# Kernel optimization log

Measured on AMD Instinct MI355X. Metric: run time of the kernel, lower is better.

## Reference

```python
import jax, jax.numpy as jnp
import numpy as np

NEG_SLOPE = 0.2  # DGL GATConv default negative_slope


def gat_conv(x, W, attn_l, attn_r, bias, src, dst, n_nodes):
    """DGL-style GATConv. x:[N,F_in], W:[F_in,H*D], attn_l/attn_r/bias:[H,D].
    Returns [N,H,D]."""
    H, D = attn_l.shape
    feat = (x @ W).reshape(n_nodes, H, D)            # projected features
    el = jnp.sum(feat * attn_l, axis=-1)              # [N,H]
    er = jnp.sum(feat * attn_r, axis=-1)              # [N,H]
    e = jax.nn.leaky_relu(el[src] + er[dst], NEG_SLOPE)  # [E,H] per-edge score
    # edge softmax over incoming edges of each dst node (numerically stable)
    m = jax.ops.segment_max(e, dst, num_segments=n_nodes)   # [N,H]
    a = jnp.exp(e - m[dst])
    denom = jax.ops.segment_sum(a, dst, num_segments=n_nodes)
    alpha = a / denom[dst]                            # [E,H]
    msg = feat[src] * alpha[..., None]                # [E,H,D]
    out = jax.ops.segment_sum(msg, dst, num_segments=n_nodes)  # [N,H,D]
    return out + bias


def setup_inputs() -> dict:
    key = jax.random.key(0)
    ks = jax.random.split(key, 12)
    N, E = 50000, 800000
    F_in, D1, H1, F_out = 128, 32, 4, 64
    h = jax.random.normal(ks[0], (N, F_in), dtype=jnp.float32)
    src = jax.random.randint(ks[1], (E,), 0, N, dtype=jnp.int32)
    dst = jax.random.randint(ks[2], (E,), 0, N, dtype=jnp.int32)
    s1 = 1.0 / np.sqrt(F_in)
    s2 = 1.0 / np.sqrt(H1 * D1)
    W1 = jax.random.normal(ks[3], (F_in, H1 * D1), dtype=jnp.float32) * s1
    al1 = jax.random.normal(ks[4], (H1, D1), dtype=jnp.float32) * s1
    ar1 = jax.random.normal(ks[5], (H1, D1), dtype=jnp.float32) * s1
    b1 = jnp.zeros((H1, D1), dtype=jnp.float32)
    W2 = jax.random.normal(ks[6], (H1 * D1, 1 * F_out), dtype=jnp.float32) * s2
    al2 = jax.random.normal(ks[7], (1, F_out), dtype=jnp.float32) * s2
    ar2 = jax.random.normal(ks[8], (1, F_out), dtype=jnp.float32) * s2
    b2 = jnp.zeros((1, F_out), dtype=jnp.float32)
    return {"h": h, "src": src, "dst": dst,
            "W1": W1, "al1": al1, "ar1": ar1, "b1": b1,
            "W2": W2, "al2": al2, "ar2": ar2, "b2": b2}


def reference(h, src, dst, W1, al1, ar1, b1, W2, al2, ar2, b2):
    N = h.shape[0]
    x = gat_conv(h, W1, al1, ar1, b1, src, dst, N)   # [N,H,D]
    x = jax.nn.relu(x.reshape(N, -1))                # flatten heads + ReLU
    # dropout(p=0.2) is identity in eval mode
    x = gat_conv(x, W2, al2, ar2, b2, src, dst, N)   # [N,1,F_out]
    return x.squeeze(1)
```

## Files before the change

kernel.cpp:

```cpp
#include <hip/hip_runtime.h>

#define NEG_SLOPE 0.2f
#define CH 4096
#define DCAP 2048
#define BSTRIDE 1536

__device__ inline unsigned short f2bf(float f) {
    unsigned u = __float_as_uint(f);
    unsigned r = (u + 0x7FFFu + ((u >> 16) & 1u)) >> 16;
    return (unsigned short)r;
}
__device__ inline unsigned pack2bf(float a, float b) {
    return (unsigned)f2bf(a) | ((unsigned)f2bf(b) << 16);
}
__device__ inline float bf2f(unsigned short s) {
    return __uint_as_float(((unsigned)s) << 16);
}
__device__ inline float bf2f_lo(unsigned u) { return __uint_as_float(u << 16); }
__device__ inline float bf2f_hi(unsigned u) { return __uint_as_float(u & 0xFFFF0000u); }
__device__ inline void wave_lds_fence() {
    asm volatile("s_waitcnt lgkmcnt(0)" ::: "memory");
}

__global__ __launch_bounds__(256) void csrP_gemm1_kernel(
    const int* __restrict__ src, const int* __restrict__ dst,
    int* __restrict__ bucket_cursor, unsigned* __restrict__ tmp, int E, int NB,
    int nchunks, const float* __restrict__ h, const float* __restrict__ W1,
    const float* __restrict__ al1, const float* __restrict__ ar1,
    unsigned short* __restrict__ feat1b, float* __restrict__ el1,
    float* __restrict__ er1, int N) {
    __shared__ __align__(16) int smem[8192];
    const int tid = threadIdx.x;
    if ((int)blockIdx.x < nchunks) {
        int* lh = smem;
        int* lex = smem + 1024;
        int* gbase_sh = smem + 2048;
        int* psum = smem + 3072;
        unsigned* sortedv = (unsigned*)(smem + 3328);
        const int base_e = blockIdx.x * CH;
        const int cnt_e = min(CH, E - base_e);
        for (int i = tid; i < 1024; i += 256) lh[i] = 0;
        __syncthreads();
        for (int i = tid; i < cnt_e; i += 256) atomicAdd(&lh[dst[base_e + i] >> 6], 1);
        __syncthreads();
        int s0 = lh[tid * 4], s1 = lh[tid * 4 + 1], s2 = lh[tid * 4 + 2],
            s3 = lh[tid * 4 + 3];
        int tot = s0 + s1 + s2 + s3;
        psum[tid] = tot;
        __syncthreads();
        for (int off = 1; off < 256; off <<= 1) {
            int t = (tid >= off) ? psum[tid - off] : 0;
            __syncthreads();
            psum[tid] += t;
            __syncthreads();
        }
        int ebase = psum[tid] - tot;
        lex[tid * 4] = ebase;
        lex[tid * 4 + 1] = ebase + s0;
        lex[tid * 4 + 2] = ebase + s0 + s1;
        lex[tid * 4 + 3] = ebase + s0 + s1 + s2;
        for (int b = tid; b < NB; b += 256) {
            int c = lh[b];
            gbase_sh[b] = c ? atomicAdd(&bucket_cursor[b], c) : 0;
        }
        __syncthreads();
        for (int i = tid; i < 1024; i += 256) lh[i] = 0;
        __syncthreads();
        for (int i = tid; i < cnt_e; i += 256) {
            int e = base_e + i;
            int d = dst[e];
            unsigned b = (unsigned)d >> 6;
            int r = atomicAdd(&lh[b], 1);
            sortedv[lex[b] + r] =
                (b << 22) | ((unsigned)(d & 63) << 16) | (unsigned)(src[e] & 0xFFFF);
        }
        __syncthreads();
        for (int i = tid; i < cnt_e; i += 256) {
            unsigned v = sortedv[i];
            int b = v >> 22;
            int pos = gbase_sh[b] + (i - lex[b]);
            if (pos < BSTRIDE)
                tmp[(size_t)b * BSTRIDE + pos] = v;
        }
    } else {
        float* xs = (float*)smem;
        const int row0 = ((int)blockIdx.x - nchunks) * 64;
        {
            const float4* s4 = (const float4*)h;
            float4* d4 = (float4*)xs;
            int base4 = row0 * 32;
            int tot4 = N * 32;
            for (int i = tid; i < 2048; i += 256)
                if (base4 + i < tot4) d4[i] = s4[base4 + i];
        }
        __syncthreads();
        const int lane = tid & 31;
        const int c0 = lane * 4;
        const int r0 = (tid >> 5) * 8;
        float acc[8][4] = {};
#pragma unroll 4
        for (int k = 0; k < 128; ++k) {
            float4 w = *(const float4*)(W1 + k * 128 + c0);
#pragma unroll
            for (int r = 0; r < 8; ++r) {
                float x = xs[(r0 + r) * 128 + k];
                acc[r][0] = fmaf(x, w.x, acc[r][0]);
                acc[r][1] = fmaf(x, w.y, acc[r][1]);
                acc[r][2] = fmaf(x, w.z, acc[r][2]);
                acc[r][3] = fmaf(x, w.w, acc[r][3]);
            }
        }
        float4 alv = *(const float4*)(al1 + c0);
        float4 arv = *(const float4*)(ar1 + c0);
#pragma unroll
        for (int r = 0; r < 8; ++r) {
            int row = row0 + r0 + r;
            if (row < N) {
                ushort4 fb;
                fb.x = f2bf(acc[r][0]);
                fb.y = f2bf(acc[r][1]);
                fb.z = f2bf(acc[r][2]);
                fb.w = f2bf(acc[r][3]);
                *(ushort4*)(feat1b + (size_t)row * 128 + c0) = fb;
                float pl = acc[r][0] * alv.x + acc[r][1] * alv.y + acc[r][2] * alv.z +
                           acc[r][3] * alv.w;
                float pr = acc[r][0] * arv.x + acc[r][1] * arv.y + acc[r][2] * arv.z +
                           acc[r][3] * arv.w;
#pragma unroll
                for (int off = 4; off >= 1; off >>= 1) {
                    pl += __shfl_xor(pl, off, 32);
                    pr += __shfl_xor(pr, off, 32);
                }
                if ((lane & 7) == 0) {
                    el1[row * 4 + (lane >> 3)] = pl;
                    er1[row * 4 + (lane >> 3)] = pr;
                }
            }
        }
    }
}

__global__ __launch_bounds__(256) void bucketD_kernel(const unsigned* __restrict__ tmp,
                                                      const int* __restrict__ bucket_cursor,
                                                      int* __restrict__ srcs,
                                                      int* __restrict__ row_beg,
                                                      int* __restrict__ row_end, int N) {
    __shared__ unsigned sval[DCAP];
    __shared__ int ssrc[DCAP];
    __shared__ int dh[64], dex[64], dcur[64];
    const int b = blockIdx.x;
    const int tid = threadIdx.x;
    const int gb = b * BSTRIDE;
    const int cnt = min(bucket_cursor[b], BSTRIDE);
    if (tid < 64) dh[tid] = 0;
    __syncthreads();
    for (int i = tid; i < cnt; i += 256) {
        unsigned v = tmp[gb + i];
        sval[i] = v;
        atomicAdd(&dh[(v >> 16) & 63], 1);
    }
    __syncthreads();
    if (tid < 64) {
        int v = dh[tid], inc = v;
        for (int off = 1; off < 64; off <<= 1) {
            int t = __shfl_up(inc, off, 64);
            if (tid >= off) inc += t;
        }
        dex[tid] = inc - v;
        dcur[tid] = 0;
        int dglob = b * 64 + tid;
        if (dglob < N) {
            row_beg[dglob] = gb + inc - v;
            row_end[dglob] = gb + inc;
        }
    }
    __syncthreads();
    for (int i = tid; i < cnt; i += 256) {
        unsigned val = sval[i];
        int dl = (val >> 16) & 63;
        int r = atomicAdd(&dcur[dl], 1);
        ssrc[dex[dl] + r] = (int)(val & 0xFFFFu);
    }
    __syncthreads();
    for (int i = tid; i < cnt; i += 256) srcs[gb + i] = ssrc[i];
}

__global__ __launch_bounds__(256) void gemm2_fused(const unsigned short* __restrict__ out1b,
                                                   const float* __restrict__ W2,
                                                   const float* __restrict__ al2,
                                                   const float* __restrict__ ar2,
                                                   unsigned short* __restrict__ feat2b,
                                                   float* __restrict__ el2,
                                                   float* __restrict__ er2, int N) {
    __shared__ float xs[64 * 128];
    const int tid = threadIdx.x;
    const int row0 = blockIdx.x * 64;
    {
        const uint4* s8 = (const uint4*)out1b;
        int base8 = row0 * 16;
        int tot8 = N * 16;
        for (int i = tid; i < 1024; i += 256)
            if (base8 + i < tot8) {
                uint4 v = s8[base8 + i];
                float* o = xs + i * 8;
                o[0] = bf2f_lo(v.x);
                o[1] = bf2f_hi(v.x);
                o[2] = bf2f_lo(v.y);
                o[3] = bf2f_hi(v.y);
                o[4] = bf2f_lo(v.z);
                o[5] = bf2f_hi(v.z);
                o[6] = bf2f_lo(v.w);
                o[7] = bf2f_hi(v.w);
            }
    }
    __syncthreads();
    const int lane = tid & 15;
    const int c0 = lane * 4;
    const int r0 = (tid >> 4) * 4;
    float acc[4][4] = {};
#pragma unroll 4
    for (int k = 0; k < 128; ++k) {
        float4 w = *(const float4*)(W2 + k * 64 + c0);
#pragma unroll
        for (int r = 0; r < 4; ++r) {
            float x = xs[(r0 + r) * 128 + k];
            acc[r][0] = fmaf(x, w.x, acc[r][0]);
            acc[r][1] = fmaf(x, w.y, acc[r][1]);
            acc[r][2] = fmaf(x, w.z, acc[r][2]);
            acc[r][3] = fmaf(x, w.w, acc[r][3]);
        }
    }
    float4 alv = *(const float4*)(al2 + c0);
    float4 arv = *(const float4*)(ar2 + c0);
#pragma unroll
    for (int r = 0; r < 4; ++r) {
        int row = row0 + r0 + r;
        if (row < N) {
            ushort4 fb;
            fb.x = f2bf(acc[r][0]);
            fb.y = f2bf(acc[r][1]);
            fb.z = f2bf(acc[r][2]);
            fb.w = f2bf(acc[r][3]);
            *(ushort4*)(feat2b + (size_t)row * 64 + c0) = fb;
            float pl = acc[r][0] * alv.x + acc[r][1] * alv.y + acc[r][2] * alv.z +
                       acc[r][3] * alv.w;
            float pr = acc[r][0] * arv.x + acc[r][1] * arv.y + acc[r][2] * arv.z +
                       acc[r][3] * arv.w;
#pragma unroll
            for (int off = 8; off >= 1; off >>= 1) {
                pl += __shfl_xor(pl, off, 16);
                pr += __shfl_xor(pr, off, 16);
            }
            if (lane == 0) {
                el2[row] = pl;
                er2[row] = pr;
            }
        }
    }
}

__global__ __launch_bounds__(256) void gather1_kernel(const int* __restrict__ row_beg,
                                                      const int* __restrict__ row_end,
                                                      const int* __restrict__ srcs,
                                                      const float* __restrict__ el1,
                                                      const float* __restrict__ er1,
                                                      const unsigned short* __restrict__ feat1b,
                                                      const float* __restrict__ b1,
                                                      unsigned short* __restrict__ out1b,
                                                      int N) {
    __shared__ int s_sh[4][64];
    __shared__ float a_sh[4][256];
    const int tid = threadIdx.x;
    const int w = tid >> 6;
    const int lane = tid & 63;
    const int d = blockIdx.x * 4 + w;
    if (d >= N) return;
    const int beg = row_beg[d], end = row_end[d];
    const int q = lane >> 4;
    const int l16 = lane & 15;
    const int c0 = l16 * 8;
    const int h = l16 >> 2;
    float4 er4 = *(const float4*)(er1 + (size_t)d * 4);
    float acc[8] = {}, bcc[8] = {};
    float den = 0.f;
    for (int k0 = beg; k0 < end; k0 += 64) {
        const int M = min(64, end - k0);
        if (lane < M) {
            int s = srcs[k0 + lane];
            s_sh[w][lane] = s;
            float4 el4 = *(const float4*)(el1 + (size_t)s * 4);
            float v0 = el4.x + er4.x;
            float v1 = el4.y + er4.y;
            float v2 = el4.z + er4.z;
            float v3 = el4.w + er4.w;
            v0 = v0 > 0.f ? v0 : NEG_SLOPE * v0;
            v1 = v1 > 0.f ? v1 : NEG_SLOPE * v1;
            v2 = v2 > 0.f ? v2 : NEG_SLOPE * v2;
            v3 = v3 > 0.f ? v3 : NEG_SLOPE * v3;
            a_sh[w][lane * 4 + 0] = __expf(v0);
            a_sh[w][lane * 4 + 1] = __expf(v1);
            a_sh[w][lane * 4 + 2] = __expf(v2);
            a_sh[w][lane * 4 + 3] = __expf(v3);
        }
        wave_lds_fence();
        int e = q;
        for (; e + 4 < M; e += 8) {
            int s0 = s_sh[w][e], s1 = s_sh[w][e + 4];
            float a0 = a_sh[w][e * 4 + h];
            float a1 = a_sh[w][(e + 4) * 4 + h];
            uint4 f0 = *(const uint4*)(feat1b + (size_t)s0 * 128 + c0);
            uint4 f1 = *(const uint4*)(feat1b + (size_t)s1 * 128 + c0);
            den += a0 + a1;
            acc[0] = fmaf(bf2f_lo(f0.x), a0, acc[0]);
            acc[1] = fmaf(bf2f_hi(f0.x), a0, acc[1]);
            acc[2] = fmaf(bf2f_lo(f0.y), a0, acc[2]);
            acc[3] = fmaf(bf2f_hi(f0.y), a0, acc[3]);
            acc[4] = fmaf(bf2f_lo(f0.z), a0, acc[4]);
            acc[5] = fmaf(bf2f_hi(f0.z), a0, acc[5]);
            acc[6] = fmaf(bf2f_lo(f0.w), a0, acc[6]);
            acc[7] = fmaf(bf2f_hi(f0.w), a0, acc[7]);
            bcc[0] = fmaf(bf2f_lo(f1.x), a1, bcc[0]);
            bcc[1] = fmaf(bf2f_hi(f1.x), a1, bcc[1]);
            bcc[2] = fmaf(bf2f_lo(f1.y), a1, bcc[2]);
            bcc[3] = fmaf(bf2f_hi(f1.y), a1, bcc[3]);
            bcc[4] = fmaf(bf2f_lo(f1.z), a1, bcc[4]);
            bcc[5] = fmaf(bf2f_hi(f1.z), a1, bcc[5]);
            bcc[6] = fmaf(bf2f_lo(f1.w), a1, bcc[6]);
            bcc[7] = fmaf(bf2f_hi(f1.w), a1, bcc[7]);
        }
        while (e < M) {
            int s0 = s_sh[w][e];
            float a0 = a_sh[w][e * 4 + h];
            uint4 f0 = *(const uint4*)(feat1b + (size_t)s0 * 128 + c0);
            den += a0;
            acc[0] = fmaf(bf2f_lo(f0.x), a0, acc[0]);
            acc[1] = fmaf(bf2f_hi(f0.x), a0, acc[1]);
            acc[2] = fmaf(bf2f_lo(f0.y), a0, acc[2]);
            acc[3] = fmaf(bf2f_hi(f0.y), a0, acc[3]);
            acc[4] = fmaf(bf2f_lo(f0.z), a0, acc[4]);
            acc[5] = fmaf(bf2f_hi(f0.z), a0, acc[5]);
            acc[6] = fmaf(bf2f_lo(f0.w), a0, acc[6]);
            acc[7] = fmaf(bf2f_hi(f0.w), a0, acc[7]);
            e += 4;
        }
        wave_lds_fence();
    }
#pragma unroll
    for (int j = 0; j < 8; ++j) {
        acc[j] += bcc[j];
        acc[j] += __shfl_xor(acc[j], 16, 64);
        acc[j] += __shfl_xor(acc[j], 32, 64);
    }
    den += __shfl_xor(den, 16, 64);
    den += __shfl_xor(den, 32, 64);
    if (q == 0) {
        float inv = (end > beg) ? 1.f / den : 0.f;
        float4 bv0 = *(const float4*)(b1 + c0);
        float4 bv1 = *(const float4*)(b1 + c0 + 4);
        uint4 o;
        o.x = pack2bf(fmaxf(acc[0] * inv + bv0.x, 0.f), fmaxf(acc[1] * inv + bv0.y, 0.f));
        o.y = pack2bf(fmaxf(acc[2] * inv + bv0.z, 0.f), fmaxf(acc[3] * inv + bv0.w, 0.f));
        o.z = pack2bf(fmaxf(acc[4] * inv + bv1.x, 0.f), fmaxf(acc[5] * inv + bv1.y, 0.f));
        o.w = pack2bf(fmaxf(acc[6] * inv + bv1.z, 0.f), fmaxf(acc[7] * inv + bv1.w, 0.f));
        *(uint4*)(out1b + (size_t)d * 128 + c0) = o;
    }
}

__global__ __launch_bounds__(256) void gather2_kernel(const int* __restrict__ row_beg,
                                                      const int* __restrict__ row_end,
                                                      const int* __restrict__ srcs,
                                                      const float* __restrict__ el2,
                                                      const float* __restrict__ er2,
                                                      const unsigned short* __restrict__ feat2b,
                                                      const float* __restrict__ b2,
                                                      float* __restrict__ out2, int N) {
    __shared__ int s_sh[4][64];
    __shared__ float a_sh[4][64];
    const int tid = threadIdx.x;
    const int w = tid >> 6;
    const int lane = tid & 63;
    const int d = blockIdx.x * 4 + w;
    if (d >= N) return;
    const int beg = row_beg[d], end = row_end[d];
    const int oct = lane >> 3;
    const int l8 = lane & 7;
    const int c0 = l8 * 8;
    const float er_d = er2[d];
    float acc[8] = {}, bcc[8] = {};
    float den = 0.f;
    for (int k0 = beg; k0 < end; k0 += 64) {
        const int M = min(64, end - k0);
        if (lane < M) {
            int s = srcs[k0 + lane];
            s_sh[w][lane] = s;
            float v = el2[s] + er_d;
            v = v > 0.f ? v : NEG_SLOPE * v;
            a_sh[w][lane] = __expf(v);
        }
        wave_lds_fence();
        int e = oct;
        for (; e + 8 < M; e += 16) {
            int s0 = s_sh[w][e], s1 = s_sh[w][e + 8];
            float a0 = a_sh[w][e], a1 = a_sh[w][e + 8];
            uint4 f0 = *(const uint4*)(feat2b + (size_t)s0 * 64 + c0);
            uint4 f1 = *(const uint4*)(feat2b + (size_t)s1 * 64 + c0);
            den += a0 + a1;
            acc[0] = fmaf(bf2f_lo(f0.x), a0, acc[0]);
            acc[1] = fmaf(bf2f_hi(f0.x), a0, acc[1]);
            acc[2] = fmaf(bf2f_lo(f0.y), a0, acc[2]);
            acc[3] = fmaf(bf2f_hi(f0.y), a0, acc[3]);
            acc[4] = fmaf(bf2f_lo(f0.z), a0, acc[4]);
            acc[5] = fmaf(bf2f_hi(f0.z), a0, acc[5]);
            acc[6] = fmaf(bf2f_lo(f0.w), a0, acc[6]);
            acc[7] = fmaf(bf2f_hi(f0.w), a0, acc[7]);
            bcc[0] = fmaf(bf2f_lo(f1.x), a1, bcc[0]);
            bcc[1] = fmaf(bf2f_hi(f1.x), a1, bcc[1]);
            bcc[2] = fmaf(bf2f_lo(f1.y), a1, bcc[2]);
            bcc[3] = fmaf(bf2f_hi(f1.y), a1, bcc[3]);
            bcc[4] = fmaf(bf2f_lo(f1.z), a1, bcc[4]);
            bcc[5] = fmaf(bf2f_hi(f1.z), a1, bcc[5]);
            bcc[6] = fmaf(bf2f_lo(f1.w), a1, bcc[6]);
            bcc[7] = fmaf(bf2f_hi(f1.w), a1, bcc[7]);
        }
        while (e < M) {
            int s0 = s_sh[w][e];
            float a0 = a_sh[w][e];
            uint4 f0 = *(const uint4*)(feat2b + (size_t)s0 * 64 + c0);
            den += a0;
            acc[0] = fmaf(bf2f_lo(f0.x), a0, acc[0]);
            acc[1] = fmaf(bf2f_hi(f0.x), a0, acc[1]);
            acc[2] = fmaf(bf2f_lo(f0.y), a0, acc[2]);
            acc[3] = fmaf(bf2f_hi(f0.y), a0, acc[3]);
            acc[4] = fmaf(bf2f_lo(f0.z), a0, acc[4]);
            acc[5] = fmaf(bf2f_hi(f0.z), a0, acc[5]);
            acc[6] = fmaf(bf2f_lo(f0.w), a0, acc[6]);
            acc[7] = fmaf(bf2f_hi(f0.w), a0, acc[7]);
            e += 8;
        }
        wave_lds_fence();
    }
#pragma unroll
    for (int j = 0; j < 8; ++j) {
        acc[j] += bcc[j];
        acc[j] += __shfl_xor(acc[j], 8, 64);
        acc[j] += __shfl_xor(acc[j], 16, 64);
        acc[j] += __shfl_xor(acc[j], 32, 64);
    }
    den += __shfl_xor(den, 8, 64);
    den += __shfl_xor(den, 16, 64);
    den += __shfl_xor(den, 32, 64);
    if (oct == 0) {
        float inv = (end > beg) ? 1.f / den : 0.f;
        float4 bv0 = *(const float4*)(b2 + c0);
        float4 bv1 = *(const float4*)(b2 + c0 + 4);
        *(float4*)(out2 + (size_t)d * 64 + c0) =
            make_float4(acc[0] * inv + bv0.x, acc[1] * inv + bv0.y,
                        acc[2] * inv + bv0.z, acc[3] * inv + bv0.w);
        *(float4*)(out2 + (size_t)d * 64 + c0 + 4) =
            make_float4(acc[4] * inv + bv1.x, acc[5] * inv + bv1.y,
                        acc[6] * inv + bv1.z, acc[7] * inv + bv1.w);
    }
}

extern "C" void kernel_launch(void* const* d_in, const int* in_sizes, int n_in,
                              void* d_out, int out_size, void* d_ws, size_t ws_size,
                              hipStream_t stream) {
    const float* h   = (const float*)d_in[0];
    const int*   src = (const int*)d_in[1];
    const int*   dst = (const int*)d_in[2];
    const float* W1  = (const float*)d_in[3];
    const float* al1 = (const float*)d_in[4];
    const float* ar1 = (const float*)d_in[5];
    const float* b1  = (const float*)d_in[6];
    const float* W2  = (const float*)d_in[7];
    const float* al2 = (const float*)d_in[8];
    const float* ar2 = (const float*)d_in[9];
    const float* b2  = (const float*)d_in[10];

    const int N = in_sizes[0] / 128;
    const int E = in_sizes[1];
    const int NB = (N + 63) >> 6;

    char* ws = (char*)d_ws;
    size_t off = 0;
    auto alloc = [&](size_t elems) -> void* {
        void* p = (void*)(ws + off);
        off += ((elems * 4 + 255) / 256) * 256;
        return p;
    };
    int* bucket_cursor = (int*)alloc(NB);
    unsigned* tmp      = (unsigned*)alloc((size_t)NB * BSTRIDE);
    int* srcs          = (int*)alloc((size_t)NB * BSTRIDE);
    int* row_beg       = (int*)alloc(N);
    int* row_end       = (int*)alloc(N);
    float* el1   = (float*)alloc((size_t)N * 4);
    float* er1   = (float*)alloc((size_t)N * 4);
    unsigned short* feat1b = (unsigned short*)alloc((size_t)N * 64);
    unsigned short* out1b  = (unsigned short*)alloc((size_t)N * 64);
    float* el2   = (float*)alloc(N);
    float* er2   = (float*)alloc(N);
    unsigned short* feat2b = (unsigned short*)alloc((size_t)N * 32);
    float* out2  = (float*)d_out;

    const int nchunks = (E + CH - 1) / CH;
    const int gemm1_blocks = (N + 63) / 64;

    hipMemsetAsync(bucket_cursor, 0, (size_t)NB * 4, stream);
    csrP_gemm1_kernel<<<nchunks + gemm1_blocks, 256, 0, stream>>>(
        src, dst, bucket_cursor, tmp, E, NB, nchunks, h, W1, al1, ar1, feat1b,
        el1, er1, N);
    bucketD_kernel<<<NB, 256, 0, stream>>>(tmp, bucket_cursor, srcs, row_beg,
                                           row_end, N);

    gather1_kernel<<<(N + 3) / 4, 256, 0, stream>>>(row_beg, row_end, srcs, el1,
                                                    er1, feat1b, b1, out1b, N);

    gemm2_fused<<<(N + 63) / 64, 256, 0, stream>>>(out1b, W2, al2, ar2, feat2b, el2,
                                                   er2, N);
    gather2_kernel<<<(N + 3) / 4, 256, 0, stream>>>(row_beg, row_end, srcs, el2,
                                                    er2, feat2b, b2, out2, N);
}
```

Before: 213.6 us.

## Fuse per-bucket CSR sort into both gather kernels, drop bucketD pass

Removes the separate bucketD kernel and the global srcs/row_beg/row_end arrays. Each gather kernel now loads its bucket's packed edges from tmp and does the per-destination counting sort in LDS, then processes 32 destinations per block (8 per wave). The block-level prefix scan in the first kernel also switches from a barrier-heavy LDS scan to wave shuffles plus a per-wave sum. The cost is that the bucket sort is redone in each gather kernel, and the grid has far fewer blocks with heavier work each and larger LDS use.

```diff
diff --git a/kernel.cpp b/kernel.cpp
--- a/kernel.cpp
+++ b/kernel.cpp
@@ -2,7 +2,6 @@
 
 #define NEG_SLOPE 0.2f
 #define CH 4096
-#define DCAP 2048
 #define BSTRIDE 1536
 
 __device__ inline unsigned short f2bf(float f) {
@@ -12,9 +11,6 @@
 }
 __device__ inline unsigned pack2bf(float a, float b) {
     return (unsigned)f2bf(a) | ((unsigned)f2bf(b) << 16);
-}
-__device__ inline float bf2f(unsigned short s) {
-    return __uint_as_float(((unsigned)s) << 16);
 }
 __device__ inline float bf2f_lo(unsigned u) { return __uint_as_float(u << 16); }
 __device__ inline float bf2f_hi(unsigned u) { return __uint_as_float(u & 0xFFFF0000u); }
@@ -35,26 +31,32 @@
         int* lh = smem;
         int* lex = smem + 1024;
         int* gbase_sh = smem + 2048;
-        int* psum = smem + 3072;
-        unsigned* sortedv = (unsigned*)(smem + 3328);
+        int* wsum = smem + 3072;
+        unsigned* sortedv = (unsigned*)(smem + 3104);
         const int base_e = blockIdx.x * CH;
         const int cnt_e = min(CH, E - base_e);
         for (int i = tid; i < 1024; i += 256) lh[i] = 0;
         __syncthreads();
         for (int i = tid; i < cnt_e; i += 256) atomicAdd(&lh[dst[base_e + i] >> 6], 1);
         __syncthreads();
+        const int lane = tid & 63;
+        const int wid = tid >> 6;
         int s0 = lh[tid * 4], s1 = lh[tid * 4 + 1], s2 = lh[tid * 4 + 2],
             s3 = lh[tid * 4 + 3];
         int tot = s0 + s1 + s2 + s3;
-        psum[tid] = tot;
-        __syncthreads();
-        for (int off = 1; off < 256; off <<= 1) {
-            int t = (tid >= off) ? psum[tid - off] : 0;
-            __syncthreads();
-            psum[tid] += t;
-            __syncthreads();
-        }
-        int ebase = psum[tid] - tot;
+        int inc = tot;
+#pragma unroll
+        for (int off = 1; off < 64; off <<= 1) {
+            int t = __shfl_up(inc, off, 64);
+            if (lane >= off) inc += t;
+        }
+        if (lane == 63) wsum[wid] = inc;
+        __syncthreads();
+        int wbase = 0;
+#pragma unroll
+        for (int k = 0; k < 4; ++k)
+            if (k < wid) wbase += wsum[k];
+        int ebase = wbase + inc - tot;
         lex[tid * 4] = ebase;
         lex[tid * 4 + 1] = ebase + s0;
         lex[tid * 4 + 2] = ebase + s0 + s1;
@@ -138,51 +140,6 @@
             }
         }
     }
-}
-
-__global__ __launch_bounds__(256) void bucketD_kernel(const unsigned* __restrict__ tmp,
-                                                      const int* __restrict__ bucket_cursor,
-                                                      int* __restrict__ srcs,
-                                                      int* __restrict__ row_beg,
-                                                      int* __restrict__ row_end, int N) {
-    __shared__ unsigned sval[DCAP];
-    __shared__ int ssrc[DCAP];
-    __shared__ int dh[64], dex[64], dcur[64];
-    const int b = blockIdx.x;
-    const int tid = threadIdx.x;
-    const int gb = b * BSTRIDE;
-    const int cnt = min(bucket_cursor[b], BSTRIDE);
-    if (tid < 64) dh[tid] = 0;
-    __syncthreads();
-    for (int i = tid; i < cnt; i += 256) {
-        unsigned v = tmp[gb + i];
-        sval[i] = v;
-        atomicAdd(&dh[(v >> 16) & 63], 1);
-    }
-    __syncthreads();
-    if (tid < 64) {
-        int v = dh[tid], inc = v;
-        for (int off = 1; off < 64; off <<= 1) {
-            int t = __shfl_up(inc, off, 64);
-            if (tid >= off) inc += t;
-        }
-        dex[tid] = inc - v;
-        dcur[tid] = 0;
-        int dglob = b * 64 + tid;
-        if (dglob < N) {
-            row_beg[dglob] = gb + inc - v;
-            row_end[dglob] = gb + inc;
-        }
-    }
-    __syncthreads();
-    for (int i = tid; i < cnt; i += 256) {
-        unsigned val = sval[i];
-        int dl = (val >> 16) & 63;
-        int r = atomicAdd(&dcur[dl], 1);
-        ssrc[dex[dl] + r] = (int)(val & 0xFFFFu);
-    }
-    __syncthreads();
-    for (int i = tid; i < cnt; i += 256) srcs[gb + i] = ssrc[i];
 }
 
 __global__ __launch_bounds__(256) void gemm2_fused(const unsigned short* __restrict__ out1b,
@@ -259,206 +216,274 @@
     }
 }
 
-__global__ __launch_bounds__(256) void gather1_kernel(const int* __restrict__ row_beg,
-                                                      const int* __restrict__ row_end,
-                                                      const int* __restrict__ srcs,
+__global__ __launch_bounds__(256) void gather1_kernel(const unsigned* __restrict__ tmp,
+                                                      const int* __restrict__ bucket_cursor,
                                                       const float* __restrict__ el1,
                                                       const float* __restrict__ er1,
                                                       const unsigned short* __restrict__ feat1b,
                                                       const float* __restrict__ b1,
                                                       unsigned short* __restrict__ out1b,
                                                       int N) {
-    __shared__ int s_sh[4][64];
+    __shared__ unsigned sval[BSTRIDE];
+    __shared__ int ssrc[BSTRIDE];
+    __shared__ int dh[64], dex[64], dcur[64];
     __shared__ float a_sh[4][256];
     const int tid = threadIdx.x;
+    const int b = (int)blockIdx.x >> 1;
+    const int half = (int)blockIdx.x & 1;
+    const int gb = b * BSTRIDE;
+    const int cnt = min(bucket_cursor[b], BSTRIDE);
+    if (tid < 64) dh[tid] = 0;
+    __syncthreads();
+    for (int i = tid; i < cnt; i += 256) {
+        unsigned v = tmp[gb + i];
+        sval[i] = v;
+        atomicAdd(&dh[(v >> 16) & 63], 1);
+    }
+    __syncthreads();
+    if (tid < 64) {
+        int v = dh[tid], inc = v;
+#pragma unroll
+        for (int off = 1; off < 64; off <<= 1) {
+            int t = __shfl_up(inc, off, 64);
+            if (tid >= off) inc += t;
+        }
+        dex[tid] = inc - v;
+        dcur[tid] = inc - v;
+    }
+    __syncthreads();
+    for (int i = tid; i < cnt; i += 256) {
+        unsigned val = sval[i];
+        int dl = (val >> 16) & 63;
+        int pos = atomicAdd(&dcur[dl], 1);
+        ssrc[pos] = (int)(val & 0xFFFFu);
+    }
+    __syncthreads();
     const int w = tid >> 6;
     const int lane = tid & 63;
-    const int d = blockIdx.x * 4 + w;
-    if (d >= N) return;
-    const int beg = row_beg[d], end = row_end[d];
     const int q = lane >> 4;
     const int l16 = lane & 15;
     const int c0 = l16 * 8;
-    const int h = l16 >> 2;
-    float4 er4 = *(const float4*)(er1 + (size_t)d * 4);
-    float acc[8] = {}, bcc[8] = {};
-    float den = 0.f;
-    for (int k0 = beg; k0 < end; k0 += 64) {
-        const int M = min(64, end - k0);
-        if (lane < M) {
-            int s = srcs[k0 + lane];
-            s_sh[w][lane] = s;
-            float4 el4 = *(const float4*)(el1 + (size_t)s * 4);
-            float v0 = el4.x + er4.x;
-            float v1 = el4.y + er4.y;
-            float v2 = el4.z + er4.z;
-            float v3 = el4.w + er4.w;
-            v0 = v0 > 0.f ? v0 : NEG_SLOPE * v0;
-            v1 = v1 > 0.f ? v1 : NEG_SLOPE * v1;
-            v2 = v2 > 0.f ? v2 : NEG_SLOPE * v2;
-            v3 = v3 > 0.f ? v3 : NEG_SLOPE * v3;
-            a_sh[w][lane * 4 + 0] = __expf(v0);
-            a_sh[w][lane * 4 + 1] = __expf(v1);
-            a_sh[w][lane * 4 + 2] = __expf(v2);
-            a_sh[w][lane * 4 + 3] = __expf(v3);
-        }
-        wave_lds_fence();
-        int e = q;
-        for (; e + 4 < M; e += 8) {
-            int s0 = s_sh[w][e], s1 = s_sh[w][e + 4];
-            float a0 = a_sh[w][e * 4 + h];
-            float a1 = a_sh[w][(e + 4) * 4 + h];
-            uint4 f0 = *(const uint4*)(feat1b + (size_t)s0 * 128 + c0);
-            uint4 f1 = *(const uint4*)(feat1b + (size_t)s1 * 128 + c0);
-            den += a0 + a1;
-            acc[0] = fmaf(bf2f_lo(f0.x), a0, acc[0]);
-            acc[1] = fmaf(bf2f_hi(f0.x), a0, acc[1]);
-            acc[2] = fmaf(bf2f_lo(f0.y), a0, acc[2]);
-            acc[3] = fmaf(bf2f_hi(f0.y), a0, acc[3]);
-            acc[4] = fmaf(bf2f_lo(f0.z), a0, acc[4]);
-            acc[5] = fmaf(bf2f_hi(f0.z), a0, acc[5]);
-            acc[6] = fmaf(bf2f_lo(f0.w), a0, acc[6]);
-            acc[7] = fmaf(bf2f_hi(f0.w), a0, acc[7]);
-            bcc[0] = fmaf(bf2f_lo(f1.x), a1, bcc[0]);
-            bcc[1] = fmaf(bf2f_hi(f1.x), a1, bcc[1]);
-            bcc[2] = fmaf(bf2f_lo(f1.y), a1, bcc[2]);
-            bcc[3] = fmaf(bf2f_hi(f1.y), a1, bcc[3]);
-            bcc[4] = fmaf(bf2f_lo(f1.z), a1, bcc[4]);
-            bcc[5] = fmaf(bf2f_hi(f1.z), a1, bcc[5]);
-            bcc[6] = fmaf(bf2f_lo(f1.w), a1, bcc[6]);
-            bcc[7] = fmaf(bf2f_hi(f1.w), a1, bcc[7]);
-        }
-        while (e < M) {
-            int s0 = s_sh[w][e];
-            float a0 = a_sh[w][e * 4 + h];
-            uint4 f0 = *(const uint4*)(feat1b + (size_t)s0 * 128 + c0);
-            den += a0;
-            acc[0] = fmaf(bf2f_lo(f0.x), a0, acc[0]);
-            acc[1] = fmaf(bf2f_hi(f0.x), a0, acc[1]);
-            acc[2] = fmaf(bf2f_lo(f0.y), a0, acc[2]);
-            acc[3] = fmaf(bf2f_hi(f0.y), a0, acc[3]);
-            acc[4] = fmaf(bf2f_lo(f0.z), a0, acc[4]);
-            acc[5] = fmaf(bf2f_hi(f0.z), a0, acc[5]);
-            acc[6] = fmaf(bf2f_lo(f0.w), a0, acc[6]);
-            acc[7] = fmaf(bf2f_hi(f0.w), a0, acc[7]);
-            e += 4;
-        }
-        wave_lds_fence();
-    }
-#pragma unroll
-    for (int j = 0; j < 8; ++j) {
-        acc[j] += bcc[j];
-        acc[j] += __shfl_xor(acc[j], 16, 64);
-        acc[j] += __shfl_xor(acc[j], 32, 64);
-    }
-    den += __shfl_xor(den, 16, 64);
-    den += __shfl_xor(den, 32, 64);
-    if (q == 0) {
-        float inv = (end > beg) ? 1.f / den : 0.f;
-        float4 bv0 = *(const float4*)(b1 + c0);
-        float4 bv1 = *(const float4*)(b1 + c0 + 4);
-        uint4 o;
-        o.x = pack2bf(fmaxf(acc[0] * inv + bv0.x, 0.f), fmaxf(acc[1] * inv + bv0.y, 0.f));
-        o.y = pack2bf(fmaxf(acc[2] * inv + bv0.z, 0.f), fmaxf(acc[3] * inv + bv0.w, 0.f));
-        o.z = pack2bf(fmaxf(acc[4] * inv + bv1.x, 0.f), fmaxf(acc[5] * inv + bv1.y, 0.f));
-        o.w = pack2bf(fmaxf(acc[6] * inv + bv1.z, 0.f), fmaxf(acc[7] * inv + bv1.w, 0.f));
-        *(uint4*)(out1b + (size_t)d * 128 + c0) = o;
-    }
-}
-
-__global__ __launch_bounds__(256) void gather2_kernel(const int* __restrict__ row_beg,
-                                                      const int* __restrict__ row_end,
-                                                      const int* __restrict__ srcs,
+    const int hh = l16 >> 2;
+    float4 bv0 = *(const float4*)(b1 + c0);
+    float4 bv1 = *(const float4*)(b1 + c0 + 4);
+    for (int k = 0; k < 8; ++k) {
+        const int dl = half * 32 + w * 8 + k;
+        const int d = b * 64 + dl;
+        if (d >= N) break;
+        const int base = dex[dl];
+        const int M = dh[dl];
+        float4 er4 = *(const float4*)(er1 + (size_t)d * 4);
+        float acc[8] = {}, bcc[8] = {};
+        float den = 0.f;
+        for (int k0 = 0; k0 < M; k0 += 64) {
+            const int Mt = min(64, M - k0);
+            if (lane < Mt) {
+                int s = ssrc[base + k0 + lane];
+                float4 el4 = *(const float4*)(el1 + (size_t)s * 4);
+                float v0 = el4.x + er4.x;
+                float v1 = el4.y + er4.y;
+                float v2 = el4.z + er4.z;
+                float v3 = el4.w + er4.w;
+                v0 = v0 > 0.f ? v0 : NEG_SLOPE * v0;
+                v1 = v1 > 0.f ? v1 : NEG_SLOPE * v1;
+                v2 = v2 > 0.f ? v2 : NEG_SLOPE * v2;
+                v3 = v3 > 0.f ? v3 : NEG_SLOPE * v3;
+                a_sh[w][lane * 4 + 0] = __expf(v0);
+                a_sh[w][lane * 4 + 1] = __expf(v1);
+                a_sh[w][lane * 4 + 2] = __expf(v2);
+                a_sh[w][lane * 4 + 3] = __expf(v3);
+            }
+            wave_lds_fence();
+            int e = q;
+            for (; e + 4 < Mt; e += 8) {
+                int s0 = ssrc[base + k0 + e], s1 = ssrc[base + k0 + e + 4];
+                float a0 = a_sh[w][e * 4 + hh];
+                float a1 = a_sh[w][(e + 4) * 4 + hh];
+                uint4 f0 = *(const uint4*)(feat1b + (size_t)s0 * 128 + c0);
+                uint4 f1 = *(const uint4*)(feat1b + (size_t)s1 * 128 + c0);
+                den += a0 + a1;
+                acc[0] = fmaf(bf2f_lo(f0.x), a0, acc[0]);
+                acc[1] = fmaf(bf2f_hi(f0.x), a0, acc[1]);
+                acc[2] = fmaf(bf2f_lo(f0.y), a0, acc[2]);
+                acc[3] = fmaf(bf2f_hi(f0.y), a0, acc[3]);
+                acc[4] = fmaf(bf2f_lo(f0.z), a0, acc[4]);
+                acc[5] = fmaf(bf2f_hi(f0.z), a0, acc[5]);
+                acc[6] = fmaf(bf2f_lo(f0.w), a0, acc[6]);
+                acc[7] = fmaf(bf2f_hi(f0.w), a0, acc[7]);
+                bcc[0] = fmaf(bf2f_lo(f1.x), a1, bcc[0]);
+                bcc[1] = fmaf(bf2f_hi(f1.x), a1, bcc[1]);
+                bcc[2] = fmaf(bf2f_lo(f1.y), a1, bcc[2]);
+                bcc[3] = fmaf(bf2f_hi(f1.y), a1, bcc[3]);
+                bcc[4] = fmaf(bf2f_lo(f1.z), a1, bcc[4]);
+                bcc[5] = fmaf(bf2f_hi(f1.z), a1, bcc[5]);
+                bcc[6] = fmaf(bf2f_lo(f1.w), a1, bcc[6]);
+                bcc[7] = fmaf(bf2f_hi(f1.w), a1, bcc[7]);
+            }
+            while (e < Mt) {
+                int s0 = ssrc[base + k0 + e];
+                float a0 = a_sh[w][e * 4 + hh];
+                uint4 f0 = *(const uint4*)(feat1b + (size_t)s0 * 128 + c0);
+                den += a0;
+                acc[0] = fmaf(bf2f_lo(f0.x), a0, acc[0]);
+                acc[1] = fmaf(bf2f_hi(f0.x), a0, acc[1]);
+                acc[2] = fmaf(bf2f_lo(f0.y), a0, acc[2]);
+                acc[3] = fmaf(bf2f_hi(f0.y), a0, acc[3]);
+                acc[4] = fmaf(bf2f_lo(f0.z), a0, acc[4]);
+                acc[5] = fmaf(bf2f_hi(f0.z), a0, acc[5]);
+                acc[6] = fmaf(bf2f_lo(f0.w), a0, acc[6]);
+                acc[7] = fmaf(bf2f_hi(f0.w), a0, acc[7]);
+                e += 4;
+            }
+            wave_lds_fence();
+        }
+#pragma unroll
+        for (int j = 0; j < 8; ++j) {
+            acc[j] += bcc[j];
+            acc[j] += __shfl_xor(acc[j], 16, 64);
+            acc[j] += __shfl_xor(acc[j], 32, 64);
+        }
+        den += __shfl_xor(den, 16, 64);
+        den += __shfl_xor(den, 32, 64);
+        if (q == 0) {
+            float inv = (M > 0) ? 1.f / den : 0.f;
+            uint4 o;
+            o.x = pack2bf(fmaxf(acc[0] * inv + bv0.x, 0.f), fmaxf(acc[1] * inv + bv0.y, 0.f));
+            o.y = pack2bf(fmaxf(acc[2] * inv + bv0.z, 0.f), fmaxf(acc[3] * inv + bv0.w, 0.f));
+            o.z = pack2bf(fmaxf(acc[4] * inv + bv1.x, 0.f), fmaxf(acc[5] * inv + bv1.y, 0.f));
+            o.w = pack2bf(fmaxf(acc[6] * inv + bv1.z, 0.f), fmaxf(acc[7] * inv + bv1.w, 0.f));
+            *(uint4*)(out1b + (size_t)d * 128 + c0) = o;
+        }
+    }
+}
+
+__global__ __launch_bounds__(256) void gather2_kernel(const unsigned* __restrict__ tmp,
+                                                      const int* __restrict__ bucket_cursor,
                                                       const float* __restrict__ el2,
                                                       const float* __restrict__ er2,
                                                       const unsigned short* __restrict__ feat2b,
                                                       const float* __restrict__ b2,
                                                       float* __restrict__ out2, int N) {
-    __shared__ int s_sh[4][64];
+    __shared__ unsigned sval[BSTRIDE];
+    __shared__ int ssrc[BSTRIDE];
+    __shared__ int dh[64], dex[64], dcur[64];
     __shared__ float a_sh[4][64];
     const int tid = threadIdx.x;
+    const int b = (int)blockIdx.x >> 1;
+    const int half = (int)blockIdx.x & 1;
+    const int gb = b * BSTRIDE;
+    const int cnt = min(bucket_cursor[b], BSTRIDE);
+    if (tid < 64) dh[tid] = 0;
+    __syncthreads();
+    for (int i = tid; i < cnt; i += 256) {
+        unsigned v = tmp[gb + i];
+        sval[i] = v;
+        atomicAdd(&dh[(v >> 16) & 63], 1);
+    }
+    __syncthreads();
+    if (tid < 64) {
+        int v = dh[tid], inc = v;
+#pragma unroll
+        for (int off = 1; off < 64; off <<= 1) {
+            int t = __shfl_up(inc, off, 64);
+            if (tid >= off) inc += t;
+        }
+        dex[tid] = inc - v;
+        dcur[tid] = inc - v;
+    }
+    __syncthreads();
+    for (int i = tid; i < cnt; i += 256) {
+        unsigned val = sval[i];
+        int dl = (val >> 16) & 63;
+        int pos = atomicAdd(&dcur[dl], 1);
+        ssrc[pos] = (int)(val & 0xFFFFu);
+    }
+    __syncthreads();
     const int w = tid >> 6;
     const int lane = tid & 63;
-    const int d = blockIdx.x * 4 + w;
-    if (d >= N) return;
-    const int beg = row_beg[d], end = row_end[d];
     const int oct = lane >> 3;
     const int l8 = lane & 7;
     const int c0 = l8 * 8;
-    const float er_d = er2[d];
-    float acc[8] = {}, bcc[8] = {};
-    float den = 0.f;
-    for (int k0 = beg; k0 < end; k0 += 64) {
-        const int M = min(64, end - k0);
-        if (lane < M) {
-            int s = srcs[k0 + lane];
-            s_sh[w][lane] = s;
-            float v = el2[s] + er_d;
-            v = v > 0.f ? v : NEG_SLOPE * v;
-            a_sh[w][lane] = __expf(v);
-        }
-        wave_lds_fence();
-        int e = oct;
-        for (; e + 8 < M; e += 16) {
-            int s0 = s_sh[w][e], s1 = s_sh[w][e + 8];
-            float a0 = a_sh[w][e], a1 = a_sh[w][e + 8];
-            uint4 f0 = *(const uint4*)(feat2b + (size_t)s0 * 64 + c0);
-            uint4 f1 = *(const uint4*)(feat2b + (size_t)s1 * 64 + c0);
-            den += a0 + a1;
-            acc[0] = fmaf(bf2f_lo(f0.x), a0, acc[0]);
-            acc[1] = fmaf(bf2f_hi(f0.x), a0, acc[1]);
-            acc[2] = fmaf(bf2f_lo(f0.y), a0, acc[2]);
-            acc[3] = fmaf(bf2f_hi(f0.y), a0, acc[3]);
-            acc[4] = fmaf(bf2f_lo(f0.z), a0, acc[4]);
-            acc[5] = fmaf(bf2f_hi(f0.z), a0, acc[5]);
-            acc[6] = fmaf(bf2f_lo(f0.w), a0, acc[6]);
-            acc[7] = fmaf(bf2f_hi(f0.w), a0, acc[7]);
-            bcc[0] = fmaf(bf2f_lo(f1.x), a1, bcc[0]);
-            bcc[1] = fmaf(bf2f_hi(f1.x), a1, bcc[1]);
-            bcc[2] = fmaf(bf2f_lo(f1.y), a1, bcc[2]);
-            bcc[3] = fmaf(bf2f_hi(f1.y), a1, bcc[3]);
-            bcc[4] = fmaf(bf2f_lo(f1.z), a1, bcc[4]);
-            bcc[5] = fmaf(bf2f_hi(f1.z), a1, bcc[5]);
-            bcc[6] = fmaf(bf2f_lo(f1.w), a1, bcc[6]);
-            bcc[7] = fmaf(bf2f_hi(f1.w), a1, bcc[7]);
-        }
-        while (e < M) {
-            int s0 = s_sh[w][e];
-            float a0 = a_sh[w][e];
-            uint4 f0 = *(const uint4*)(feat2b + (size_t)s0 * 64 + c0);
-            den += a0;
-            acc[0] = fmaf(bf2f_lo(f0.x), a0, acc[0]);
-            acc[1] = fmaf(bf2f_hi(f0.x), a0, acc[1]);
-            acc[2] = fmaf(bf2f_lo(f0.y), a0, acc[2]);
-            acc[3] = fmaf(bf2f_hi(f0.y), a0, acc[3]);
-            acc[4] = fmaf(bf2f_lo(f0.z), a0, acc[4]);
-            acc[5] = fmaf(bf2f_hi(f0.z), a0, acc[5]);
-            acc[6] = fmaf(bf2f_lo(f0.w), a0, acc[6]);
-            acc[7] = fmaf(bf2f_hi(f0.w), a0, acc[7]);
-            e += 8;
-        }
-        wave_lds_fence();
-    }
-#pragma unroll
-    for (int j = 0; j < 8; ++j) {
-        acc[j] += bcc[j];
-        acc[j] += __shfl_xor(acc[j], 8, 64);
-        acc[j] += __shfl_xor(acc[j], 16, 64);
-        acc[j] += __shfl_xor(acc[j], 32, 64);
-    }
-    den += __shfl_xor(den, 8, 64);
-    den += __shfl_xor(den, 16, 64);
-    den += __shfl_xor(den, 32, 64);
-    if (oct == 0) {
-        float inv = (end > beg) ? 1.f / den : 0.f;
-        float4 bv0 = *(const float4*)(b2 + c0);
-        float4 bv1 = *(const float4*)(b2 + c0 + 4);
-        *(float4*)(out2 + (size_t)d * 64 + c0) =
-            make_float4(acc[0] * inv + bv0.x, acc[1] * inv + bv0.y,
-                        acc[2] * inv + bv0.z, acc[3] * inv + bv0.w);
-        *(float4*)(out2 + (size_t)d * 64 + c0 + 4) =
-            make_float4(acc[4] * inv + bv1.x, acc[5] * inv + bv1.y,
-                        acc[6] * inv + bv1.z, acc[7] * inv + bv1.w);
+    float4 bv0 = *(const float4*)(b2 + c0);
+    float4 bv1 = *(const float4*)(b2 + c0 + 4);
+    for (int k = 0; k < 8; ++k) {
+        const int dl = half * 32 + w * 8 + k;
+        const int d = b * 64 + dl;
+        if (d >= N) break;
+        const int base = dex[dl];
+        const int M = dh[dl];
+        const float er_d = er2[d];
+        float acc[8] = {}, bcc[8] = {};
+        float den = 0.f;
+        for (int k0 = 0; k0 < M; k0 += 64) {
+            const int Mt = min(64, M - k0);
+            if (lane < Mt) {
+                int s = ssrc[base + k0 + lane];
+                float v = el2[s] + er_d;
+                v = v > 0.f ? v : NEG_SLOPE * v;
+                a_sh[w][lane] = __expf(v);
+            }
+            wave_lds_fence();
+            int e = oct;
+            for (; e + 8 < Mt; e += 16) {
+                int s0 = ssrc[base + k0 + e], s1 = ssrc[base + k0 + e + 8];
+                float a0 = a_sh[w][e], a1 = a_sh[w][e + 8];
+                uint4 f0 = *(const uint4*)(feat2b + (size_t)s0 * 64 + c0);
+                uint4 f1 = *(const uint4*)(feat2b + (size_t)s1 * 64 + c0);
+                den += a0 + a1;
+                acc[0] = fmaf(bf2f_lo(f0.x), a0, acc[0]);
+                acc[1] = fmaf(bf2f_hi(f0.x), a0, acc[1]);
+                acc[2] = fmaf(bf2f_lo(f0.y), a0, acc[2]);
+                acc[3] = fmaf(bf2f_hi(f0.y), a0, acc[3]);
+                acc[4] = fmaf(bf2f_lo(f0.z), a0, acc[4]);
+                acc[5] = fmaf(bf2f_hi(f0.z), a0, acc[5]);
+                acc[6] = fmaf(bf2f_lo(f0.w), a0, acc[6]);
+                acc[7] = fmaf(bf2f_hi(f0.w), a0, acc[7]);
+                bcc[0] = fmaf(bf2f_lo(f1.x), a1, bcc[0]);
+                bcc[1] = fmaf(bf2f_hi(f1.x), a1, bcc[1]);
+                bcc[2] = fmaf(bf2f_lo(f1.y), a1, bcc[2]);
+                bcc[3] = fmaf(bf2f_hi(f1.y), a1, bcc[3]);
+                bcc[4] = fmaf(bf2f_lo(f1.z), a1, bcc[4]);
+                bcc[5] = fmaf(bf2f_hi(f1.z), a1, bcc[5]);
+                bcc[6] = fmaf(bf2f_lo(f1.w), a1, bcc[6]);
+                bcc[7] = fmaf(bf2f_hi(f1.w), a1, bcc[7]);
+            }
+            while (e < Mt) {
+                int s0 = ssrc[base + k0 + e];
+                float a0 = a_sh[w][e];
+                uint4 f0 = *(const uint4*)(feat2b + (size_t)s0 * 64 + c0);
+                den += a0;
+                acc[0] = fmaf(bf2f_lo(f0.x), a0, acc[0]);
+                acc[1] = fmaf(bf2f_hi(f0.x), a0, acc[1]);
+                acc[2] = fmaf(bf2f_lo(f0.y), a0, acc[2]);
+                acc[3] = fmaf(bf2f_hi(f0.y), a0, acc[3]);
+                acc[4] = fmaf(bf2f_lo(f0.z), a0, acc[4]);
+                acc[5] = fmaf(bf2f_hi(f0.z), a0, acc[5]);
+                acc[6] = fmaf(bf2f_lo(f0.w), a0, acc[6]);
+                acc[7] = fmaf(bf2f_hi(f0.w), a0, acc[7]);
+                e += 8;
+            }
+            wave_lds_fence();
+        }
+#pragma unroll
+        for (int j = 0; j < 8; ++j) {
+            acc[j] += bcc[j];
+            acc[j] += __shfl_xor(acc[j], 8, 64);
+            acc[j] += __shfl_xor(acc[j], 16, 64);
+            acc[j] += __shfl_xor(acc[j], 32, 64);
+        }
+        den += __shfl_xor(den, 8, 64);
+        den += __shfl_xor(den, 16, 64);
+        den += __shfl_xor(den, 32, 64);
+        if (oct == 0) {
+            float inv = (M > 0) ? 1.f / den : 0.f;
+            *(float4*)(out2 + (size_t)d * 64 + c0) =
+                make_float4(acc[0] * inv + bv0.x, acc[1] * inv + bv0.y,
+                            acc[2] * inv + bv0.z, acc[3] * inv + bv0.w);
+            *(float4*)(out2 + (size_t)d * 64 + c0 + 4) =
+                make_float4(acc[4] * inv + bv1.x, acc[5] * inv + bv1.y,
+                            acc[6] * inv + bv1.z, acc[7] * inv + bv1.w);
+        }
     }
 }
 
@@ -490,9 +515,6 @@
     };
     int* bucket_cursor = (int*)alloc(NB);
     unsigned* tmp      = (unsigned*)alloc((size_t)NB * BSTRIDE);
-    int* srcs          = (int*)alloc((size_t)NB * BSTRIDE);
-    int* row_beg       = (int*)alloc(N);
-    int* row_end       = (int*)alloc(N);
     float* el1   = (float*)alloc((size_t)N * 4);
     float* er1   = (float*)alloc((size_t)N * 4);
     unsigned short* feat1b = (unsigned short*)alloc((size_t)N * 64);
@@ -509,14 +531,12 @@
     csrP_gemm1_kernel<<<nchunks + gemm1_blocks, 256, 0, stream>>>(
         src, dst, bucket_cursor, tmp, E, NB, nchunks, h, W1, al1, ar1, feat1b,
         el1, er1, N);
-    bucketD_kernel<<<NB, 256, 0, stream>>>(tmp, bucket_cursor, srcs, row_beg,
-                                           row_end, N);
-
-    gather1_kernel<<<(N + 3) / 4, 256, 0, stream>>>(row_beg, row_end, srcs, el1,
-                                                    er1, feat1b, b1, out1b, N);
+
+    gather1_kernel<<<NB * 2, 256, 0, stream>>>(tmp, bucket_cursor, el1, er1,
+                                               feat1b, b1, out1b, N);
 
     gemm2_fused<<<(N + 63) / 64, 256, 0, stream>>>(out1b, W2, al2, ar2, feat2b, el2,
                                                    er2, N);
-    gather2_kernel<<<(N + 3) / 4, 256, 0, stream>>>(row_beg, row_end, srcs, el2,
-                                                    er2, feat2b, b2, out2, N);
-}
+    gather2_kernel<<<NB * 2, 256, 0, stream>>>(tmp, bucket_cursor, el2, er2,
+                                               feat2b, b2, out2, N);
+}
```

Result: no change. 209.5 us (-1.9%).
